# Kernel tuning notes

Hardware: AMD Instinct MI355X
Metric: run time of the kernel (lower is better)

## Reference

```python
import jax, jax.numpy as jnp
import numpy as np
import math

B, S, H = 2, 1024, 768
NH = 12
DH = H // NH  # 64


def _heads(t):
    # (B,S,H) -> (B,NH,S,DH)
    b, s, _ = t.shape
    return t.reshape(b, s, NH, DH).transpose(0, 2, 1, 3)


def _merge(t):
    # (B,NH,S,DH) -> (B,S,H)
    b, nh, s, dh = t.shape
    return t.transpose(0, 2, 1, 3).reshape(b, s, nh * dh)


def _forward(x, y, vq_w, vq_b, vk_w, vk_b, vv_w, vv_b,
             dq_w, dq_b, dk_w, dk_b, dv_w, dv_b,
             van_fc_w, van_fc_b, WD_w, d_theta_w, d_theta_b, WV_w,
             diff_fc_w, diff_fc_b, v_gamma_w, v_gamma_b,
             diff_out_w, diff_out_b, van_out_w, van_out_b,
             diff_fus_w, diff_fus_b, van_fus_w, van_fus_b,
             gate_w, nf_w, nf_b, nf_out_w, final_w, final_b):
    scale = 1.0 / math.sqrt(DH)

    # ---- Vanilla attention (dropout is eval-mode identity) ----
    q = _heads(x @ vq_w + vq_b)
    k = _heads(y @ vk_w + vk_b)
    v = _heads(y @ vv_w + vv_b)
    scores = jnp.einsum('bhid,bhjd->bhij', q, k) * scale
    probs = jax.nn.softmax(scores, axis=-1)
    van_vector = _merge(jnp.einsum('bhij,bhjd->bhid', probs, v))

    # ---- Differential attention ----
    # scores[b,h,i,j] = sum_d (q[b,h,i,d] - k[b,h,i,d]) / sqrt(DH)  (constant over j,
    # due to the module's broadcast indexing). Keep explicit softmax for exact math/vjp.
    dq = _heads(x @ dq_w + dq_b)
    dk = _heads(y @ dk_w + dk_b)
    dv = _heads(y @ dv_w + dv_b)
    s_row = (dq.sum(-1) - dk.sum(-1)) * scale  # (B,NH,S)
    d_scores = jnp.broadcast_to(s_row[..., None], s_row.shape + (s_row.shape[-1],))
    d_probs = jax.nn.softmax(d_scores, axis=-1)
    diff_vector = _merge(jnp.einsum('bhij,bhjd->bhid', d_probs, dv))

    # ---- Coupled gating (SoftMax over dim=1 == sequence axis) ----
    theta = jnp.tanh(jnp.concatenate((diff_vector @ WD_w, x_lin(van_vector, van_fc_w, van_fc_b)), axis=-1))
    d_theta = diff_vector * jax.nn.softmax(theta @ d_theta_w + d_theta_b, axis=1)
    gamma = jnp.tanh(jnp.concatenate((van_vector @ WV_w, d_theta @ diff_fc_w + diff_fc_b), axis=-1))
    a_gamma = van_vector * jax.nn.softmax(gamma @ v_gamma_w + v_gamma_b, axis=1)
    diff_out = jnp.tanh(jnp.concatenate((diff_vector, d_theta), axis=-1) @ diff_out_w + diff_out_b)
    van_out = jnp.tanh(jnp.concatenate((van_vector, a_gamma), axis=-1) @ van_out_w + van_out_b)
    diff_fusion = jnp.tanh(diff_out @ diff_fus_w + diff_fus_b)
    van_fusion = jnp.tanh(van_out @ van_fus_w + van_fus_b)
    gate = jax.nn.sigmoid(jnp.concatenate((diff_fusion, van_fusion), axis=-1) @ gate_w)  # (B,S,1)
    fusion = gate * van_fusion + (1.0 - gate) * diff_fusion
    nf = jax.nn.sigmoid(jnp.concatenate((van_vector, fusion @ nf_w + nf_b), axis=-1) @ nf_out_w)
    return nf * jnp.tanh(fusion @ final_w + final_b)


def x_lin(t, w, b):
    return t @ w + b


def setup_inputs() -> dict:
    key = jax.random.key(0)
    ks = iter(jax.random.split(key, 64))
    def w(*shape):
        return jax.random.normal(next(ks), shape, jnp.float32) * 0.02
    def b(n):
        return jnp.zeros((n,), jnp.float32)
    inp = {
        'x': jax.random.normal(next(ks), (B, S, H), jnp.float32),
        'y': jax.random.normal(next(ks), (B, S, H), jnp.float32),
        'vq_w': w(H, H), 'vq_b': b(H), 'vk_w': w(H, H), 'vk_b': b(H), 'vv_w': w(H, H), 'vv_b': b(H),
        'dq_w': w(H, H), 'dq_b': b(H), 'dk_w': w(H, H), 'dk_b': b(H), 'dv_w': w(H, H), 'dv_b': b(H),
        'van_fc_w': w(H, H), 'van_fc_b': b(H),
        'WD_w': w(H, H),
        'd_theta_w': w(2 * H, H), 'd_theta_b': b(H),
        'WV_w': w(H, H),
        'diff_fc_w': w(H, H), 'diff_fc_b': b(H),
        'v_gamma_w': w(2 * H, H), 'v_gamma_b': b(H),
        'diff_out_w': w(2 * H, H), 'diff_out_b': b(H),
        'van_out_w': w(2 * H, H), 'van_out_b': b(H),
        'diff_fus_w': w(H, H), 'diff_fus_b': b(H),
        'van_fus_w': w(H, H), 'van_fus_b': b(H),
        'gate_w': w(2 * H, 1),
        'nf_w': w(H, H), 'nf_b': b(H),
        'nf_out_w': w(2 * H, 1),
        'final_w': w(H, H), 'final_b': b(H),
    }
    return inp


def reference(x, y, vq_w, vq_b, vk_w, vk_b, vv_w, vv_b,
              dq_w, dq_b, dk_w, dk_b, dv_w, dv_b,
              van_fc_w, van_fc_b, WD_w, d_theta_w, d_theta_b, WV_w,
              diff_fc_w, diff_fc_b, v_gamma_w, v_gamma_b,
              diff_out_w, diff_out_b, van_out_w, van_out_b,
              diff_fus_w, diff_fus_b, van_fus_w, van_fus_b,
              gate_w, nf_w, nf_b, nf_out_w, final_w, final_b):
    return _forward(x, y, vq_w, vq_b, vk_w, vk_b, vv_w, vv_b,
                    dq_w, dq_b, dk_w, dk_b, dv_w, dv_b,
                    van_fc_w, van_fc_b, WD_w, d_theta_w, d_theta_b, WV_w,
                    diff_fc_w, diff_fc_b, v_gamma_w, v_gamma_b,
                    diff_out_w, diff_out_b, van_out_w, van_out_b,
                    diff_fus_w, diff_fus_b, van_fus_w, van_fus_b,
                    gate_w, nf_w, nf_b, nf_out_w, final_w, final_b)
```

## Files before the change

### kernel.cpp

```cpp
#include <hip/hip_runtime.h>
#include <hip/hip_bf16.h>
#include <math.h>

#define H 768
#define S 1024
#define BATCH 2
#define T 2048
#define TH ((size_t)T * H)

typedef unsigned short u16;
typedef __attribute__((ext_vector_type(8))) short short8;
typedef __attribute__((ext_vector_type(4))) float f32x4;

__device__ __forceinline__ u16 f2b(float f) {
  __hip_bfloat16 h = __float2bfloat16(f);
  return *reinterpret_cast<u16*>(&h);
}
__device__ __forceinline__ float b2f(u16 u) {
  __hip_bfloat16 h = *reinterpret_cast<__hip_bfloat16*>(&u);
  return __bfloat162float(h);
}
__device__ __forceinline__ void gload16(const u16* g, u16* lds) {
  __builtin_amdgcn_global_load_lds((const __attribute__((address_space(1))) void*)g,
                                   (__attribute__((address_space(3))) void*)lds, 16, 0, 0);
}

__global__ __launch_bounds__(256) void cvt2_k(const float* __restrict__ X, const float* __restrict__ Y,
                                              u16* __restrict__ OX, u16* __restrict__ OY) {
  const float* src = blockIdx.y ? Y : X;
  u16* dst = blockIdx.y ? OY : OX;
  int i = blockIdx.x * 256 + threadIdx.x;
  float4 a = ((const float4*)src)[2 * i];
  float4 b = ((const float4*)src)[2 * i + 1];
  u16 tmp[8] = {f2b(a.x), f2b(a.y), f2b(a.z), f2b(a.w), f2b(b.x), f2b(b.y), f2b(b.z), f2b(b.w)};
  ((uint4*)dst)[i] = *(uint4*)tmp;
}

struct WprepArgs {
  const float* src[14];
  unsigned dst[14];
  int ktiles[14];
  int tstart[15];
};
__global__ __launch_bounds__(256) void wprep_k(WprepArgs a, u16* __restrict__ wt) {
  __shared__ float sT[64][68];
  int blk = blockIdx.x;
  int mi = 0;
  while (blk >= a.tstart[mi + 1]) ++mi;
  int local = blk - a.tstart[mi];
  int kt = a.ktiles[mi];
  int tn = local / kt, tk = local % kt;
  int K = kt * 64;
  const float* W = a.src[mi];
  u16* D = wt + a.dst[mi];
  int t = threadIdx.x;
  int r = t >> 2, c = (t & 3) * 16;
  const float4* srcp = (const float4*)(W + ((size_t)(tk * 64 + r)) * H + tn * 64 + c);
  float4 v0 = srcp[0], v1 = srcp[1], v2 = srcp[2], v3 = srcp[3];
  *(float4*)&sT[r][c] = v0; *(float4*)&sT[r][c + 4] = v1;
  *(float4*)&sT[r][c + 8] = v2; *(float4*)&sT[r][c + 12] = v3;
  __syncthreads();
  int n = t >> 2, kk = (t & 3) * 16;
  u16 tmp[16];
  #pragma unroll
  for (int j = 0; j < 16; ++j) tmp[j] = f2b(sT[kk + j][n]);
  uint4* dst = (uint4*)(D + ((size_t)(tn * 64 + n)) * K + tk * 64 + kk);
  dst[0] = *(uint4*)&tmp[0];
  dst[1] = *(uint4*)&tmp[8];
}

__global__ __launch_bounds__(256) void meany1_k(const float* __restrict__ Y, float* __restrict__ part) {
  int blk = blockIdx.x;
  int b = blk / 24, r = blk % 24, cc = r / 8, sc = r % 8;
  int c = cc * 256 + threadIdx.x;
  const float* yp = Y + (size_t)b * S * H + (size_t)sc * 128 * H + c;
  float s = 0.f;
  for (int j = 0; j < 128; ++j) s += yp[(size_t)j * H];
  part[(sc * 2 + b) * H + c] = s;
}
__global__ __launch_bounds__(256) void meany2_k(const float* __restrict__ part, float* __restrict__ ybar) {
  int t = blockIdx.x * 256 + threadIdx.x;
  float s = 0.f;
  int b = t / H, c = t % H;
  #pragma unroll
  for (int sc = 0; sc < 8; ++sc) s += part[(sc * 2 + b) * H + c];
  ybar[t] = s * (1.0f / 1024.0f);
}

__global__ __launch_bounds__(256) void gemv_k(const float* __restrict__ A, const float* __restrict__ W,
                                              const float* __restrict__ bias, float* __restrict__ O, int act) {
  int gid = blockIdx.x * 4 + (threadIdx.x >> 6);
  int lane = threadIdx.x & 63;
  int b = gid / H, n = gid % H;
  const float* a = A + b * H;
  float s = 0.f;
  #pragma unroll
  for (int i = 0; i < 12; ++i) {
    int k = lane + 64 * i;
    s = fmaf(a[k], W[(size_t)k * H + n], s);
  }
  #pragma unroll
  for (int off = 32; off; off >>= 1) s += __shfl_xor(s, off);
  if (lane == 0) {
    if (bias) s += bias[n];
    if (act) s = tanhf(s);
    O[gid] = s;
  }
}

struct Reg {
  const u16 *A, *W, *A2, *W2;
  const float *bias, *perbatch;
  u16* Cb; u16* CbT; float* Cf; float* colPart;
  int ldw, ldw2;
};
struct GArgs { Reg r0, r1, r2; int act; };

__global__ __launch_bounds__(512) void bgemm_k(GArgs ga) {
  __shared__ u16 sA[3][64 * 64];
  __shared__ u16 sB[3][64 * 64];
  int t = threadIdx.x;
  int ri = blockIdx.x / 12;
  Reg R;
  if (ri == 0) R = ga.r0; else if (ri == 1) R = ga.r1; else R = ga.r2;
  int n0 = (blockIdx.x % 12) * 64;
  int m0 = blockIdx.y * 64;
  int w = t >> 6, l = t & 63, lr = l & 15, lg = l >> 4;
  int wr = (w & 3) * 16, wc = (w >> 2) * 32;

  f32x4 acc[2];
  acc[0] = (f32x4){0.f, 0.f, 0.f, 0.f};
  acc[1] = (f32x4){0.f, 0.f, 0.f, 0.f};

  int NT = R.A2 ? 24 : 12;

  auto stage = [&](int ti) {
    int bi = ti % 3;
    const u16* Aq = (ti < 12) ? R.A : R.A2;
    const u16* Wq = (ti < 12) ? R.W : R.W2;
    int ldwq = (ti < 12) ? R.ldw : R.ldw2;
    int k0 = (ti % 12) * 64;
    int rr = t >> 3, c8 = t & 7;
    gload16(Aq + (size_t)(m0 + rr) * H + k0 + 8 * (c8 ^ (rr & 7)), &sA[bi][0] + t * 8);
    gload16(Wq + (size_t)(n0 + rr) * ldwq + k0 + 8 * (c8 ^ (rr & 7)), &sB[bi][0] + t * 8);
  };

  stage(0);
  stage(1);
  for (int kt = 0; kt < NT; ++kt) {
    if (kt + 1 < NT) asm volatile("s_waitcnt vmcnt(2)" ::: "memory");
    else             asm volatile("s_waitcnt vmcnt(0)" ::: "memory");
    __builtin_amdgcn_s_barrier();
    if (kt + 2 < NT) stage(kt + 2);
    const u16* sAv = &sA[kt % 3][0];
    const u16* sBv = &sB[kt % 3][0];
    #pragma unroll
    for (int kh = 0; kh < 2; ++kh) {
      int arow = wr + lr;
      short8 af = *(const short8*)(sAv + arow * 64 + 8 * ((4 * kh + lg) ^ (arow & 7)));
      #pragma unroll
      for (int ni = 0; ni < 2; ++ni) {
        int brow = wc + 16 * ni + lr;
        short8 bf = *(const short8*)(sBv + brow * 64 + 8 * ((4 * kh + lg) ^ (brow & 7)));
        acc[ni] = __builtin_amdgcn_mfma_f32_16x16x32_bf16(af, bf, acc[ni], 0, 0, 0);
      }
    }
  }

  float ps[2] = {0.f, 0.f};
  #pragma unroll
  for (int ni = 0; ni < 2; ++ni) {
    int col = n0 + wc + 16 * ni + lr;
    u16 tmp4[4];
    #pragma unroll
    for (int reg = 0; reg < 4; ++reg) {
      int row = m0 + wr + lg * 4 + reg;
      int bb = row >> 10;
      float v = acc[ni][reg];
      if (R.bias) v += R.bias[col];
      if (R.perbatch) v += R.perbatch[bb * H + col];
      if (ga.act) v = tanhf(v);
      tmp4[reg] = f2b(v);
      if (R.Cb) R.Cb[(size_t)row * H + col] = tmp4[reg];
      if (R.Cf) R.Cf[(size_t)row * H + col] = v;
      if (R.colPart) ps[ni] += __expf(b2f(tmp4[reg]));
    }
    if (R.CbT) {
      int row0 = m0 + wr + lg * 4;
      int bb = row0 >> 10, tok = row0 & 1023, hh = col >> 6, dd = col & 63;
      *(unsigned long long*)&R.CbT[((size_t)((bb * 12 + hh) * 64 + dd)) * 1024 + tok] =
          *(unsigned long long*)tmp4;
    }
  }
  if (R.colPart) {
    #pragma unroll
    for (int ni = 0; ni < 2; ++ni) {
      float p = ps[ni];
      p += __shfl_xor(p, 16);
      p += __shfl_xor(p, 32);
      if (lg == 0) {
        int col = n0 + wc + 16 * ni + lr;
        R.colPart[(size_t)(blockIdx.y * 4 + (w & 3)) * H + col] = p;
      }
    }
  }
}

__global__ __launch_bounds__(256) void mattn_k(
    const u16* __restrict__ Q, const u16* __restrict__ Kg,
    const u16* __restrict__ VT, u16* __restrict__ O)
{
  __shared__ u16 sK[3][64 * 64];
  __shared__ u16 sV[3][64 * 64];
  __shared__ u16 sQ[64 * 64];
  __shared__ u16 sP[4 * 16 * 64];
  int t = threadIdx.x;
  int w = t >> 6, l = t & 63, lr = l & 15, lg = l >> 4;
  int blk = blockIdx.x;
  int b = blk / 192; int rem = blk % 192; int h = rem / 16; int q0 = (rem % 16) * 64;

  #pragma unroll
  for (int i = 0; i < 2; ++i) {
    int id = t + i * 256; int r = id >> 3, c = id & 7;
    uint4 v = *(const uint4*)(Q + ((size_t)(b * 1024 + q0 + r)) * H + h * 64 + 8 * c);
    *(uint4*)(&sQ[0] + r * 64 + 8 * (c ^ (r & 7))) = v;
  }

  auto stageKV = [&](int ti) {
    int bi = ti % 3;
    int kv0 = ti * 64;
    #pragma unroll
    for (int ii = 0; ii < 2; ++ii) {
      int chunk = w * 128 + ii * 64 + l;
      int rr = chunk >> 3, c8 = chunk & 7;
      gload16(Kg + ((size_t)(b * 1024 + kv0 + rr)) * H + h * 64 + 8 * (c8 ^ (rr & 7)),
              &sK[bi][0] + (w * 128 + ii * 64) * 8);
      gload16(VT + ((size_t)((b * 12 + h) * 64 + rr)) * 1024 + kv0 + 8 * (c8 ^ (rr & 7)),
              &sV[bi][0] + (w * 128 + ii * 64) * 8);
    }
  };

  stageKV(0);
  stageKV(1);
  asm volatile("s_waitcnt lgkmcnt(0)" ::: "memory");
  __builtin_amdgcn_s_barrier();
  short8 qreg[2];
  #pragma unroll
  for (int kh = 0; kh < 2; ++kh) {
    int qrow = 16 * w + lr;
    qreg[kh] = *(const short8*)(&sQ[0] + qrow * 64 + 8 * ((4 * kh + lg) ^ (qrow & 7)));
  }

  f32x4 oacc[4];
  #pragma unroll
  for (int i = 0; i < 4; ++i) oacc[i] = (f32x4){0.f, 0.f, 0.f, 0.f};
  float lsum[4] = {0.f, 0.f, 0.f, 0.f};

  for (int kt = 0; kt < 16; ++kt) {
    if (kt + 1 < 16) asm volatile("s_waitcnt vmcnt(4)" ::: "memory");
    else             asm volatile("s_waitcnt vmcnt(0)" ::: "memory");
    __builtin_amdgcn_s_barrier();
    if (kt + 2 < 16) stageKV(kt + 2);
    const u16* sKv = &sK[kt % 3][0];
    const u16* sVv = &sV[kt % 3][0];

    f32x4 sacc[4];
    #pragma unroll
    for (int i = 0; i < 4; ++i) sacc[i] = (f32x4){0.f, 0.f, 0.f, 0.f};
    #pragma unroll
    for (int kh = 0; kh < 2; ++kh) {
      #pragma unroll
      for (int ns = 0; ns < 4; ++ns) {
        int krow = 16 * ns + lr;
        short8 kf = *(const short8*)(sKv + krow * 64 + 8 * ((4 * kh + lg) ^ (krow & 7)));
        sacc[ns] = __builtin_amdgcn_mfma_f32_16x16x32_bf16(qreg[kh], kf, sacc[ns], 0, 0, 0);
      }
    }

    #pragma unroll
    for (int r = 0; r < 4; ++r) {
      int q = lg * 4 + r;
      #pragma unroll
      for (int ns = 0; ns < 4; ++ns) {
        float p = __expf(sacc[ns][r] * 0.125f);
        lsum[r] += p;
        int kv = 16 * ns + lr;
        unsigned byteoff = (unsigned)(w * 2048 + q * 128 + ((kv * 2) ^ ((q & 7) << 4)));
        *(u16*)((char*)sP + byteoff) = f2b(p);
      }
    }

    #pragma unroll
    for (int kh = 0; kh < 2; ++kh) {
      short8 pf = *(const short8*)((char*)sP + w * 2048 + lr * 128 + (((4 * kh + lg) << 4) ^ ((lr & 7) << 4)));
      #pragma unroll
      for (int ds = 0; ds < 4; ++ds) {
        int vrow = 16 * ds + lr;
        short8 vf = *(const short8*)(sVv + vrow * 64 + 8 * ((4 * kh + lg) ^ (vrow & 7)));
        oacc[ds] = __builtin_amdgcn_mfma_f32_16x16x32_bf16(pf, vf, oacc[ds], 0, 0, 0);
      }
    }
  }

  #pragma unroll
  for (int r = 0; r < 4; ++r) {
    #pragma unroll
    for (int off = 1; off < 16; off <<= 1) lsum[r] += __shfl_xor(lsum[r], off);
    float inv = 1.0f / lsum[r];
    int qrow = q0 + 16 * w + lg * 4 + r;
    #pragma unroll
    for (int ds = 0; ds < 4; ++ds) {
      int d = 16 * ds + lr;
      O[((size_t)(b * 1024 + qrow)) * H + h * 64 + d] = f2b(oacc[ds][r] * inv);
    }
  }
}

__global__ __launch_bounds__(256) void colsmA_k(
    const u16* __restrict__ Z, const float* __restrict__ part,
    const float* __restrict__ mulvec, const u16* __restrict__ mulmat, u16* __restrict__ O) {
  int blk = blockIdx.x;
  int b = blk >> 7, sc = blk & 127;
  int t = threadIdx.x;
  float s0 = 0.f, s1 = 0.f, s2 = 0.f;
  for (int i = b * 64; i < b * 64 + 64; ++i) {
    const float* pp = part + (size_t)i * H;
    s0 += pp[t]; s1 += pp[t + 256]; s2 += pp[t + 512];
  }
  float i0 = 1.0f / s0, i1 = 1.0f / s1, i2 = 1.0f / s2;
  size_t base = ((size_t)(b * 1024 + sc * 8)) * H;
  float m0 = 0.f, m1 = 0.f, m2 = 0.f;
  if (mulvec) { m0 = mulvec[b * H + t]; m1 = mulvec[b * H + t + 256]; m2 = mulvec[b * H + t + 512]; }
  #pragma unroll
  for (int j = 0; j < 8; ++j) {
    size_t row = base + (size_t)j * H;
    float e0 = __expf(b2f(Z[row + t]));
    float e1 = __expf(b2f(Z[row + t + 256]));
    float e2 = __expf(b2f(Z[row + t + 512]));
    float u0 = mulmat ? b2f(mulmat[row + t]) : m0;
    float u1 = mulmat ? b2f(mulmat[row + t + 256]) : m1;
    float u2 = mulmat ? b2f(mulmat[row + t + 512]) : m2;
    O[row + t] = f2b(u0 * e0 * i0);
    O[row + t + 256] = f2b(u1 * e1 * i1);
    O[row + t + 512] = f2b(u2 * e2 * i2);
  }
}

__global__ __launch_bounds__(256) void gatefuse_k(
    const u16* __restrict__ DF, const u16* __restrict__ VF,
    const float* __restrict__ GW, u16* __restrict__ FU)
{
  __shared__ float red[256];
  int tok = blockIdx.x;
  int t = threadIdx.x;
  const u16* df = DF + (size_t)tok * H;
  const u16* vf = VF + (size_t)tok * H;
  float dv[3], vv[3];
  float p = 0.f;
  #pragma unroll
  for (int i = 0; i < 3; ++i) {
    int c = t + i * 256;
    dv[i] = b2f(df[c]); vv[i] = b2f(vf[c]);
    p = fmaf(dv[i], GW[c], p);
    p = fmaf(vv[i], GW[H + c], p);
  }
  red[t] = p; __syncthreads();
  for (int st = 128; st; st >>= 1) { if (t < st) red[t] += red[t + st]; __syncthreads(); }
  float g = 1.0f / (1.0f + __expf(-red[0]));
  u16* fu = FU + (size_t)tok * H;
  #pragma unroll
  for (int i = 0; i < 3; ++i) {
    int c = t + i * 256;
    fu[c] = f2b(g * vv[i] + (1.0f - g) * dv[i]);
  }
}

__global__ __launch_bounds__(256) void nffinal_k(
    const u16* __restrict__ VAN, const float* __restrict__ NP,
    const float* __restrict__ NW, const float* __restrict__ FP,
    float* __restrict__ OUT)
{
  __shared__ float red[256];
  int tok = blockIdx.x;
  int t = threadIdx.x;
  const u16* va = VAN + (size_t)tok * H;
  const float* np = NP + (size_t)tok * H;
  float p = 0.f;
  #pragma unroll
  for (int i = 0; i < 3; ++i) {
    int c = t + i * 256;
    p = fmaf(b2f(va[c]), NW[c], p);
    p = fmaf(np[c], NW[H + c], p);
  }
  red[t] = p; __syncthreads();
  for (int st = 128; st; st >>= 1) { if (t < st) red[t] += red[t + st]; __syncthreads(); }
  float nf = 1.0f / (1.0f + __expf(-red[0]));
  const float* fp = FP + (size_t)tok * H;
  float* o = OUT + (size_t)tok * H;
  #pragma unroll
  for (int i = 0; i < 3; ++i) {
    int c = t + i * 256;
    o[c] = nf * tanhf(fp[c]);
  }
}

extern "C" void kernel_launch(void* const* d_in, const int* in_sizes, int n_in,
                              void* d_out, int out_size, void* d_ws, size_t ws_size,
                              hipStream_t stream) {
  const float* x        = (const float*)d_in[0];
  const float* y        = (const float*)d_in[1];
  const float* vq_w     = (const float*)d_in[2];
  const float* vq_b     = (const float*)d_in[3];
  const float* vk_w     = (const float*)d_in[4];
  const float* vk_b     = (const float*)d_in[5];
  const float* vv_w     = (const float*)d_in[6];
  const float* vv_b     = (const float*)d_in[7];
  const float* dv_w     = (const float*)d_in[12];
  const float* dv_b     = (const float*)d_in[13];
  const float* van_fc_w = (const float*)d_in[14];
  const float* van_fc_b = (const float*)d_in[15];
  const float* d_theta_w= (const float*)d_in[17];
  const float* WV_w     = (const float*)d_in[19];
  const float* diff_fc_w= (const float*)d_in[20];
  const float* diff_fc_b= (const float*)d_in[21];
  const float* v_gamma_w= (const float*)d_in[22];
  const float* diff_out_w=(const float*)d_in[24];
  const float* diff_out_b=(const float*)d_in[25];
  const float* van_out_w= (const float*)d_in[26];
  const float* van_out_b= (const float*)d_in[27];
  const float* diff_fus_w=(const float*)d_in[28];
  const float* diff_fus_b=(const float*)d_in[29];
  const float* van_fus_w= (const float*)d_in[30];
  const float* van_fus_b= (const float*)d_in[31];
  const float* gate_w   = (const float*)d_in[32];
  const float* nf_w     = (const float*)d_in[33];
  const float* nf_b     = (const float*)d_in[34];
  const float* nf_out_w = (const float*)d_in[35];
  const float* final_w  = (const float*)d_in[36];
  const float* final_b  = (const float*)d_in[37];
  float* out = (float*)d_out;

  u16* wt = (u16*)d_ws;
  const size_t HH_ = (size_t)H * H;
  const size_t HH2 = 2 * HH_;
  size_t woff[14];
  const float* wsrc[14] = {vq_w, vk_w, vv_w, van_fc_w, WV_w, diff_fc_w, diff_fus_w, van_fus_w,
                           nf_w, final_w, d_theta_w, v_gamma_w, diff_out_w, van_out_w};
  int wk[14] = {12,12,12,12,12,12,12,12,12,12, 24,24,24,24};
  size_t o = 0;
  for (int i = 0; i < 14; ++i) { woff[i] = o; o += (i < 10) ? HH_ : HH2; }
  u16* bufs = wt + o;
  u16* bX   = bufs + 0 * TH;
  u16* bY   = bufs + 1 * TH;
  u16* bQ   = bufs + 2 * TH;
  u16* bK   = bufs + 3 * TH;
  u16* bV   = bufs + 4 * TH;
  u16* bVT  = bufs + 5 * TH;
  u16* bVan = bufs + 6 * TH;
  float* F0 = (float*)(bufs + 7 * TH);
  float* F1 = F0 + TH;
  float* sm = F1 + TH;
  float* ybar  = sm;
  float* dvbar = sm + 1536;
  float* c2    = sm + 3072;
  float* part  = sm + 4608;
  float* colp  = sm + 4608 + 12288;

  WprepArgs wa;
  int ts = 0;
  for (int i = 0; i < 14; ++i) {
    wa.src[i] = wsrc[i];
    wa.dst[i] = (unsigned)woff[i];
    wa.ktiles[i] = wk[i];
    wa.tstart[i] = ts;
    ts += wk[i] * 12;
  }
  wa.tstart[14] = ts;
  wprep_k<<<ts, 256, 0, stream>>>(wa, wt);
  cvt2_k<<<dim3(TH / 8 / 256, 2), 256, 0, stream>>>(x, y, bX, bY);

  meany1_k<<<48, 256, 0, stream>>>(y, part);
  meany2_k<<<6, 256, 0, stream>>>(part, ybar);
  gemv_k<<<384, 256, 0, stream>>>(ybar, dv_w, dv_b, dvbar, 0);
  gemv_k<<<384, 256, 0, stream>>>(dvbar, diff_out_w, diff_out_b, c2, 0);

  const u16 *wt_vq = wt + woff[0], *wt_vk = wt + woff[1], *wt_vv = wt + woff[2],
            *wt_vanfc = wt + woff[3], *wt_WV = wt + woff[4], *wt_difffc = wt + woff[5],
            *wt_difffus = wt + woff[6], *wt_vanfus = wt + woff[7], *wt_nf = wt + woff[8],
            *wt_final = wt + woff[9], *wt_dtheta = wt + woff[10], *wt_vg = wt + woff[11],
            *wt_diffout = wt + woff[12], *wt_vanout = wt + woff[13];
  #define NO nullptr
  Reg RZ = {NO, NO, NO, NO, NO, NO, NO, NO, NO, NO, 0, 0};

  {
    GArgs g;
    g.r0 = {bX, wt_vq, NO, NO, vq_b, NO, bQ, NO, NO, NO, H, 0};
    g.r1 = {bY, wt_vk, NO, NO, vk_b, NO, bK, NO, NO, NO, H, 0};
    g.r2 = {bY, wt_vv, NO, NO, vv_b, NO, NO, bVT, NO, NO, H, 0};
    g.act = 0;
    bgemm_k<<<dim3(36, 32), 512, 0, stream>>>(g);
  }
  mattn_k<<<384, 256, 0, stream>>>(bQ, bK, bVT, bVan);

  {
    GArgs g;
    g.r0 = {bVan, wt_vanfc, NO, NO, van_fc_b, NO, bX, NO, NO, NO, H, 0};
    g.r1 = {bVan, wt_WV, NO, NO, NO, NO, bK, NO, NO, NO, H, 0};
    g.r2 = RZ;
    g.act = 1;
    bgemm_k<<<dim3(24, 32), 512, 0, stream>>>(g);
  }
  {
    GArgs g;
    g.r0 = {bX, wt_dtheta + H, NO, NO, NO, NO, bY, NO, NO, colp, 2 * H, 0};
    g.r1 = RZ; g.r2 = RZ;
    g.act = 0;
    bgemm_k<<<dim3(12, 32), 512, 0, stream>>>(g);
  }
  colsmA_k<<<256, 256, 0, stream>>>(bY, colp, dvbar, NO, bQ);
  {
    GArgs g;
    g.r0 = {bQ, wt_difffc, NO, NO, diff_fc_b, NO, bV, NO, NO, NO, H, 0};
    g.r1 = {bQ, wt_diffout + H, NO, NO, NO, c2, bY, NO, NO, NO, 2 * H, 0};
    g.r2 = RZ;
    g.act = 1;
    bgemm_k<<<dim3(24, 32), 512, 0, stream>>>(g);
  }
  {
    GArgs g;
    g.r0 = {bK, wt_vg, bV, wt_vg + H, NO, NO, bX, NO, NO, colp, 2 * H, 2 * H};
    g.r1 = RZ; g.r2 = RZ;
    g.act = 0;
    bgemm_k<<<dim3(12, 32), 512, 0, stream>>>(g);
  }
  colsmA_k<<<256, 256, 0, stream>>>(bX, colp, NO, bVan, bX);
  {
    GArgs g;
    g.r0 = {bVan, wt_vanout, bX, wt_vanout + H, van_out_b, NO, bK, NO, NO, NO, 2 * H, 2 * H};
    g.r1 = {bY, wt_difffus, NO, NO, diff_fus_b, NO, bQ, NO, NO, NO, H, 0};
    g.r2 = RZ;
    g.act = 1;
    bgemm_k<<<dim3(24, 32), 512, 0, stream>>>(g);
  }
  {
    GArgs g;
    g.r0 = {bK, wt_vanfus, NO, NO, van_fus_b, NO, bV, NO, NO, NO, H, 0};
    g.r1 = RZ; g.r2 = RZ;
    g.act = 1;
    bgemm_k<<<dim3(12, 32), 512, 0, stream>>>(g);
  }
  gatefuse_k<<<T, 256, 0, stream>>>(bQ, bV, gate_w, bY);
  {
    GArgs g;
    g.r0 = {bY, wt_nf, NO, NO, nf_b, NO, NO, NO, F0, NO, H, 0};
    g.r1 = {bY, wt_final, NO, NO, final_b, NO, NO, NO, F1, NO, H, 0};
    g.r2 = RZ;
    g.act = 0;
    bgemm_k<<<dim3(24, 32), 512, 0, stream>>>(g);
  }
  nffinal_k<<<T, 256, 0, stream>>>(bVan, F0, nf_out_w, F1, out);
}
```

Measured before the change: 226.3 us.

## Merge prep kernels, transpose score MFMA for vectorized P stores, add setprio

Folds the weight-transpose, input bf16 conversion and first mean-of-y reduction into one launch, removing two kernel launches and their serialization gaps. In the attention kernel, the QK^T MFMA operands are swapped so each lane holds four consecutive key scores for one query. This lets the probabilities be written to LDS as one 64-bit store instead of four scattered 16-bit stores, and the row-sum becomes a single per-lane scalar. s_setprio is also wrapped around the MFMA blocks in the GEMM and attention loops to favor matrix issue across waves.

```diff
diff --git a/kernel.cpp b/kernel.cpp
--- a/kernel.cpp
+++ b/kernel.cpp
@@ -9,6 +9,7 @@
 #define TH ((size_t)T * H)
 
 typedef unsigned short u16;
+typedef unsigned long long u64;
 typedef __attribute__((ext_vector_type(8))) short short8;
 typedef __attribute__((ext_vector_type(4))) float f32x4;
 
@@ -23,17 +24,6 @@
 __device__ __forceinline__ void gload16(const u16* g, u16* lds) {
   __builtin_amdgcn_global_load_lds((const __attribute__((address_space(1))) void*)g,
                                    (__attribute__((address_space(3))) void*)lds, 16, 0, 0);
-}
-
-__global__ __launch_bounds__(256) void cvt2_k(const float* __restrict__ X, const float* __restrict__ Y,
-                                              u16* __restrict__ OX, u16* __restrict__ OY) {
-  const float* src = blockIdx.y ? Y : X;
-  u16* dst = blockIdx.y ? OY : OX;
-  int i = blockIdx.x * 256 + threadIdx.x;
-  float4 a = ((const float4*)src)[2 * i];
-  float4 b = ((const float4*)src)[2 * i + 1];
-  u16 tmp[8] = {f2b(a.x), f2b(a.y), f2b(a.z), f2b(a.w), f2b(b.x), f2b(b.y), f2b(b.z), f2b(b.w)};
-  ((uint4*)dst)[i] = *(uint4*)tmp;
 }
 
 struct WprepArgs {
@@ -41,10 +31,36 @@
   unsigned dst[14];
   int ktiles[14];
   int tstart[15];
+  const float *x, *y;
+  u16 *bx, *by;
+  float* part;
 };
-__global__ __launch_bounds__(256) void wprep_k(WprepArgs a, u16* __restrict__ wt) {
+__global__ __launch_bounds__(256) void prep_k(WprepArgs a, u16* __restrict__ wt) {
   __shared__ float sT[64][68];
   int blk = blockIdx.x;
+  int t = threadIdx.x;
+  int ts = a.tstart[14];
+  if (blk >= ts + 1536) {
+    int bb = blk - ts - 1536;
+    int b = bb / 24, r = bb % 24, cc = r / 8, sc = r % 8;
+    int c = cc * 256 + t;
+    const float* yp = a.y + (size_t)b * S * H + (size_t)sc * 128 * H + c;
+    float s = 0.f;
+    for (int j = 0; j < 128; ++j) s += yp[(size_t)j * H];
+    a.part[(sc * 2 + b) * H + c] = s;
+    return;
+  }
+  if (blk >= ts) {
+    int bb = blk - ts;
+    const float* src = (bb < 768) ? a.x : a.y;
+    u16* dst = (bb < 768) ? a.bx : a.by;
+    int i = (bb % 768) * 256 + t;
+    float4 va = ((const float4*)src)[2 * i];
+    float4 vb = ((const float4*)src)[2 * i + 1];
+    u16 tmp[8] = {f2b(va.x), f2b(va.y), f2b(va.z), f2b(va.w), f2b(vb.x), f2b(vb.y), f2b(vb.z), f2b(vb.w)};
+    ((uint4*)dst)[i] = *(uint4*)tmp;
+    return;
+  }
   int mi = 0;
   while (blk >= a.tstart[mi + 1]) ++mi;
   int local = blk - a.tstart[mi];
@@ -53,7 +69,6 @@
   int K = kt * 64;
   const float* W = a.src[mi];
   u16* D = wt + a.dst[mi];
-  int t = threadIdx.x;
   int r = t >> 2, c = (t & 3) * 16;
   const float4* srcp = (const float4*)(W + ((size_t)(tk * 64 + r)) * H + tn * 64 + c);
   float4 v0 = srcp[0], v1 = srcp[1], v2 = srcp[2], v3 = srcp[3];
@@ -69,15 +84,6 @@
   dst[1] = *(uint4*)&tmp[8];
 }
 
-__global__ __launch_bounds__(256) void meany1_k(const float* __restrict__ Y, float* __restrict__ part) {
-  int blk = blockIdx.x;
-  int b = blk / 24, r = blk % 24, cc = r / 8, sc = r % 8;
-  int c = cc * 256 + threadIdx.x;
-  const float* yp = Y + (size_t)b * S * H + (size_t)sc * 128 * H + c;
-  float s = 0.f;
-  for (int j = 0; j < 128; ++j) s += yp[(size_t)j * H];
-  part[(sc * 2 + b) * H + c] = s;
-}
 __global__ __launch_bounds__(256) void meany2_k(const float* __restrict__ part, float* __restrict__ ybar) {
   int t = blockIdx.x * 256 + threadIdx.x;
   float s = 0.f;
@@ -154,6 +160,7 @@
     if (kt + 2 < NT) stage(kt + 2);
     const u16* sAv = &sA[kt % 3][0];
     const u16* sBv = &sB[kt % 3][0];
+    __builtin_amdgcn_s_setprio(1);
     #pragma unroll
     for (int kh = 0; kh < 2; ++kh) {
       int arow = wr + lr;
@@ -165,6 +172,7 @@
         acc[ni] = __builtin_amdgcn_mfma_f32_16x16x32_bf16(af, bf, acc[ni], 0, 0, 0);
       }
     }
+    __builtin_amdgcn_s_setprio(0);
   }
 
   float ps[2] = {0.f, 0.f};
@@ -188,8 +196,7 @@
     if (R.CbT) {
       int row0 = m0 + wr + lg * 4;
       int bb = row0 >> 10, tok = row0 & 1023, hh = col >> 6, dd = col & 63;
-      *(unsigned long long*)&R.CbT[((size_t)((bb * 12 + hh) * 64 + dd)) * 1024 + tok] =
-          *(unsigned long long*)tmp4;
+      *(u64*)&R.CbT[((size_t)((bb * 12 + hh) * 64 + dd)) * 1024 + tok] = *(u64*)tmp4;
     }
   }
   if (R.colPart) {
@@ -254,7 +261,7 @@
   f32x4 oacc[4];
   #pragma unroll
   for (int i = 0; i < 4; ++i) oacc[i] = (f32x4){0.f, 0.f, 0.f, 0.f};
-  float lsum[4] = {0.f, 0.f, 0.f, 0.f};
+  float lsum = 0.f;
 
   for (int kt = 0; kt < 16; ++kt) {
     if (kt + 1 < 16) asm volatile("s_waitcnt vmcnt(4)" ::: "memory");
@@ -267,29 +274,32 @@
     f32x4 sacc[4];
     #pragma unroll
     for (int i = 0; i < 4; ++i) sacc[i] = (f32x4){0.f, 0.f, 0.f, 0.f};
+    __builtin_amdgcn_s_setprio(1);
     #pragma unroll
     for (int kh = 0; kh < 2; ++kh) {
       #pragma unroll
       for (int ns = 0; ns < 4; ++ns) {
         int krow = 16 * ns + lr;
         short8 kf = *(const short8*)(sKv + krow * 64 + 8 * ((4 * kh + lg) ^ (krow & 7)));
-        sacc[ns] = __builtin_amdgcn_mfma_f32_16x16x32_bf16(qreg[kh], kf, sacc[ns], 0, 0, 0);
+        sacc[ns] = __builtin_amdgcn_mfma_f32_16x16x32_bf16(kf, qreg[kh], sacc[ns], 0, 0, 0);
       }
     }
-
-    #pragma unroll
-    for (int r = 0; r < 4; ++r) {
-      int q = lg * 4 + r;
+    __builtin_amdgcn_s_setprio(0);
+
+    #pragma unroll
+    for (int ns = 0; ns < 4; ++ns) {
+      u16 t4[4];
       #pragma unroll
-      for (int ns = 0; ns < 4; ++ns) {
-        float p = __expf(sacc[ns][r] * 0.125f);
-        lsum[r] += p;
-        int kv = 16 * ns + lr;
-        unsigned byteoff = (unsigned)(w * 2048 + q * 128 + ((kv * 2) ^ ((q & 7) << 4)));
-        *(u16*)((char*)sP + byteoff) = f2b(p);
+      for (int reg = 0; reg < 4; ++reg) {
+        float p = __expf(sacc[ns][reg] * 0.125f);
+        lsum += p;
+        t4[reg] = f2b(p);
       }
-    }
-
+      unsigned byteoff = (unsigned)(w * 2048 + lr * 128 + (((16 * ns + lg * 4) * 2) ^ ((lr & 7) << 4)));
+      *(u64*)((char*)sP + byteoff) = *(u64*)t4;
+    }
+
+    __builtin_amdgcn_s_setprio(1);
     #pragma unroll
     for (int kh = 0; kh < 2; ++kh) {
       short8 pf = *(const short8*)((char*)sP + w * 2048 + lr * 128 + (((4 * kh + lg) << 4) ^ ((lr & 7) << 4)));
@@ -300,13 +310,15 @@
         oacc[ds] = __builtin_amdgcn_mfma_f32_16x16x32_bf16(pf, vf, oacc[ds], 0, 0, 0);
       }
     }
-  }
-
+    __builtin_amdgcn_s_setprio(0);
+  }
+
+  lsum += __shfl_xor(lsum, 16);
+  lsum += __shfl_xor(lsum, 32);
+  float linv = 1.0f / lsum;
   #pragma unroll
   for (int r = 0; r < 4; ++r) {
-    #pragma unroll
-    for (int off = 1; off < 16; off <<= 1) lsum[r] += __shfl_xor(lsum[r], off);
-    float inv = 1.0f / lsum[r];
+    float inv = __shfl(linv, lg * 4 + r);
     int qrow = q0 + 16 * w + lg * 4 + r;
     #pragma unroll
     for (int ds = 0; ds < 4; ++ds) {
@@ -476,10 +488,9 @@
     ts += wk[i] * 12;
   }
   wa.tstart[14] = ts;
-  wprep_k<<<ts, 256, 0, stream>>>(wa, wt);
-  cvt2_k<<<dim3(TH / 8 / 256, 2), 256, 0, stream>>>(x, y, bX, bY);
-
-  meany1_k<<<48, 256, 0, stream>>>(y, part);
+  wa.x = x; wa.y = y; wa.bx = bX; wa.by = bY; wa.part = part;
+  prep_k<<<ts + 1536 + 48, 256, 0, stream>>>(wa, wt);
+
   meany2_k<<<6, 256, 0, stream>>>(part, ybar);
   gemv_k<<<384, 256, 0, stream>>>(ybar, dv_w, dv_b, dvbar, 0);
   gemv_k<<<384, 256, 0, stream>>>(dvbar, diff_out_w, diff_out_b, c2, 0);
```

New measurement: 221.5 us. -2.1%, faster.
